# Optimization experiments

Hardware: AMD Instinct MI355X
Metric: run time of the kernel (lower is better)

Reference implementation:

```python
import math
import jax, jax.numpy as jnp
import numpy as np

IMG = 64  # configs['image_size']
EPS = 1e-8


def _bilinear_matrix(in_size, out_size):
    # Matches F.interpolate(mode='bilinear', align_corners=False) exactly,
    # including clamping of negative source coords and right-edge indices.
    scale = in_size / out_size
    src = (np.arange(out_size) + 0.5) * scale - 0.5
    src = np.clip(src, 0.0, in_size - 1)
    i0 = np.floor(src).astype(np.int64)
    i1 = np.minimum(i0 + 1, in_size - 1)
    w1 = (src - i0).astype(np.float32)
    W = np.zeros((out_size, in_size), dtype=np.float32)
    W[np.arange(out_size), i0] += (1.0 - w1)
    W[np.arange(out_size), i1] += w1
    return jnp.asarray(W)


def _resize(grids, out_size):
    # grids: [B, H, W] -> [B, out, out] via separable bilinear matrices (batched matmul)
    Wh = _bilinear_matrix(grids.shape[1], out_size)
    Ww = _bilinear_matrix(grids.shape[2], out_size)
    return jnp.einsum('oh,bhw,pw->bop', Wh, grids, Ww)


def _minmax(x):
    # global min-max over the whole [B,H,W] channel tensor (as in the torch code)
    lo, hi = x.min(), x.max()
    return jnp.where(hi - lo < EPS, jnp.zeros_like(x), (x - lo) / (hi - lo + EPS))


def _to_square_grid(vec):
    # vec: [B, L] -> [B, gs, gs] with zero padding (vectorized grid scatter)
    B, L = vec.shape
    gs = int(math.ceil(math.sqrt(L)))
    return jnp.pad(vec, ((0, 0), (0, gs * gs - L))).reshape(B, gs, gs)


def setup_inputs() -> dict:
    key = jax.random.key(0)
    hidden_state = jax.random.normal(key, (64, 512, 2048, 1), dtype=jnp.float32)
    return {"hidden_state": hidden_state}


def reference(hidden_state) -> jnp.ndarray:
    xs = hidden_state[..., 0]            # [B, E, N]

    # temporal view: mean over nodes -> [B, E] -> square grid -> bilinear resize
    temporal = _minmax(_resize(_to_square_grid(xs.mean(axis=2)), IMG))

    # spatial view: mean over embedding -> [B, N] -> square grid -> resize
    spatial = _minmax(_resize(_to_square_grid(xs.mean(axis=1)), IMG))

    # correlation view: row-normalized feature correlation [B, E, E] -> resize
    xc = xs - xs.mean(axis=2, keepdims=True)
    xn = xc / (jnp.linalg.norm(xc, axis=2, keepdims=True) + EPS)
    corr = jnp.einsum('ben,bfn->bef', xn, xn)
    correlation = _minmax(_resize(corr, IMG))

    return jnp.stack([temporal, spatial, correlation], axis=1)  # [B, 3, IMG, IMG]
```

## Files before the change

kernel.cpp:

```cpp
#include <hip/hip_runtime.h>
#include <math.h>

#define B_ 64
#define E_ 512
#define N_ 2048
#define EPSF 1e-8f

#define OFF_ROWMEAN 0
#define OFF_ROWINV  32768
#define OFF_COLSUM  65536
#define OFF_MM      196608
#define OFF_RAW     196616
#define OFF_ZPART   983048

__device__ __forceinline__ unsigned mapf(float x) {
    unsigned u = __float_as_uint(x);
    return (u & 0x80000000u) ? ~u : (u | 0x80000000u);
}
__device__ __forceinline__ float unmapf(unsigned m) {
    unsigned u = (m & 0x80000000u) ? (m ^ 0x80000000u) : ~m;
    return __uint_as_float(u);
}

__global__ __launch_bounds__(256) void k_rowstats(const float* __restrict__ x,
                                                  float* __restrict__ rowmean,
                                                  float* __restrict__ rowinv) {
    int b = blockIdx.y;
    int e = blockIdx.x * 4 + (threadIdx.x >> 6);
    int lane = threadIdx.x & 63;
    const float4* row = (const float4*)(x + ((size_t)b * E_ + e) * N_);
    float s = 0.f, sq = 0.f;
#pragma unroll
    for (int i = 0; i < 8; ++i) {
        float4 v = row[lane + 64 * i];
        s  += v.x + v.y + v.z + v.w;
        sq += v.x * v.x + v.y * v.y + v.z * v.z + v.w * v.w;
    }
#pragma unroll
    for (int m = 32; m; m >>= 1) {
        s  += __shfl_xor(s, m, 64);
        sq += __shfl_xor(sq, m, 64);
    }
    if (lane == 0) {
        float mean = s * (1.0f / N_);
        float var = sq - s * s * (1.0f / N_);
        if (var < 0.f) var = 0.f;
        rowmean[b * E_ + e] = mean;
        rowinv[b * E_ + e] = 1.0f / (sqrtf(var) + EPSF);
    }
}

__global__ __launch_bounds__(256) void k_colsum(const float* __restrict__ x,
                                                float* __restrict__ colsum) {
    int b = blockIdx.y;
    int nc = blockIdx.x & 7;
    int ec = blockIdx.x >> 3;
    int n = nc * 256 + threadIdx.x;
    const float* p = x + ((size_t)b * E_ + ec * 128) * N_ + n;
    float s = 0.f;
#pragma unroll 8
    for (int e = 0; e < 128; ++e) s += p[(size_t)e * N_];
    atomicAdd(&colsum[b * N_ + n], s);
}

__global__ __launch_bounds__(256) void k_z(const float* __restrict__ x,
                                           const float* __restrict__ rowmean,
                                           const float* __restrict__ rowinv,
                                           float* __restrict__ zpart) {
    __shared__ float yt[64 * 129];
    int b = blockIdx.x;
    int s = blockIdx.y;
    int k0 = s * 128;
    int t = threadIdx.x;

    int kk = t & 127;
    int oh = t >> 7;
    for (int oo = 0; oo < 64; oo += 2) {
        int o = oo + oh;
        int r0 = 8 * o + 3, r1 = 8 * o + 4;
        float m0 = rowmean[b * E_ + r0], i0 = rowinv[b * E_ + r0];
        float m1 = rowmean[b * E_ + r1], i1 = rowinv[b * E_ + r1];
        float a = x[((size_t)b * E_ + r0) * N_ + k0 + kk];
        float c = x[((size_t)b * E_ + r1) * N_ + k0 + kk];
        yt[o * 129 + kk] = 0.5f * ((a - m0) * i0 + (c - m1) * i1);
    }
    __syncthreads();

    int ti = t >> 4, tj = t & 15;
    float acc[4][4] = {};
#pragma unroll 4
    for (int k = 0; k < 128; ++k) {
        float ai[4], aj[4];
#pragma unroll
        for (int a = 0; a < 4; ++a) ai[a] = yt[(4 * ti + a) * 129 + k];
#pragma unroll
        for (int c = 0; c < 4; ++c) aj[c] = yt[(4 * tj + c) * 129 + k];
#pragma unroll
        for (int a = 0; a < 4; ++a)
#pragma unroll
            for (int c = 0; c < 4; ++c) acc[a][c] += ai[a] * aj[c];
    }
    float* zp = zpart + ((size_t)s * B_ + b) * 4096;
#pragma unroll
    for (int a = 0; a < 4; ++a)
#pragma unroll
        for (int c = 0; c < 4; ++c)
            zp[(4 * ti + a) * 64 + (4 * tj + c)] = acc[a][c];
}

__global__ __launch_bounds__(256) void k_views(const float* __restrict__ rowmean,
                                               const float* __restrict__ colsum,
                                               const float* __restrict__ zpart,
                                               float* __restrict__ raw,
                                               unsigned* __restrict__ mm) {
    int b = blockIdx.x, v = blockIdx.y;
    int t = threadIdx.x;
    __shared__ float g[2116];
    __shared__ int   ti0[64];
    __shared__ int   ti1[64];
    __shared__ float tw[64];
    __shared__ float smin[4], smax[4];

    int gs = (v == 0) ? 23 : 46;
    if (v < 2) {
        int L = (v == 0) ? 512 : 2048;
        int gg = gs * gs;
        const float* src = (v == 0) ? (rowmean + b * E_) : (colsum + b * N_);
        float sc = (v == 0) ? 1.0f : (1.0f / 512.0f);
        for (int i = t; i < gg; i += 256) g[i] = (i < L) ? src[i] * sc : 0.f;
        if (t < 64) {
            double scd = (double)gs / 64.0;
            double sp = ((double)t + 0.5) * scd - 0.5;
            if (sp < 0.0) sp = 0.0;
            double up = (double)(gs - 1);
            if (sp > up) sp = up;
            int i0 = (int)sp;
            ti0[t] = i0;
            ti1[t] = (i0 + 1 < gs) ? i0 + 1 : gs - 1;
            tw[t] = (float)(sp - (double)i0);
        }
    }
    __syncthreads();

    float lmin = INFINITY, lmax = -INFINITY;
    for (int it = 0; it < 16; ++it) {
        int pix = t + 256 * it;
        float val;
        if (v == 2) {
            val = 0.f;
#pragma unroll
            for (int s = 0; s < 16; ++s)
                val += zpart[((size_t)s * B_ + b) * 4096 + pix];
        } else {
            int o = pix >> 6, p = pix & 63;
            int i0 = ti0[o], i1 = ti1[o];
            float wh = tw[o];
            int j0 = ti0[p], j1 = ti1[p];
            float ww = tw[p];
            float top = g[i0 * gs + j0] * (1.f - ww) + g[i0 * gs + j1] * ww;
            float bot = g[i1 * gs + j0] * (1.f - ww) + g[i1 * gs + j1] * ww;
            val = top * (1.f - wh) + bot * wh;
        }
        raw[((size_t)b * 3 + v) * 4096 + pix] = val;
        lmin = fminf(lmin, val);
        lmax = fmaxf(lmax, val);
    }

    int lane = t & 63, wid = t >> 6;
#pragma unroll
    for (int m = 32; m; m >>= 1) {
        lmin = fminf(lmin, __shfl_xor(lmin, m, 64));
        lmax = fmaxf(lmax, __shfl_xor(lmax, m, 64));
    }
    if (lane == 0) { smin[wid] = lmin; smax[wid] = lmax; }
    __syncthreads();
    if (t == 0) {
        float mn = fminf(fminf(smin[0], smin[1]), fminf(smin[2], smin[3]));
        float mx = fmaxf(fmaxf(smax[0], smax[1]), fmaxf(smax[2], smax[3]));
        atomicMin(&mm[v], mapf(mn));
        atomicMax(&mm[3 + v], mapf(mx));
    }
}

__global__ __launch_bounds__(256) void k_norm(const float* __restrict__ raw,
                                              const unsigned* __restrict__ mm,
                                              float* __restrict__ out) {
    int b = blockIdx.x, v = blockIdx.y;
    int t = threadIdx.x;
    float lo = unmapf(mm[v]);
    float hi = unmapf(mm[3 + v]);
    float d = hi - lo;
    bool zero = (d < EPSF);
    float inv = 1.0f / (d + EPSF);
    size_t base = ((size_t)b * 3 + v) * 4096;
    for (int it = 0; it < 16; ++it) {
        int pix = t + 256 * it;
        float r = raw[base + pix];
        out[base + pix] = zero ? 0.f : (r - lo) * inv;
    }
}

extern "C" void kernel_launch(void* const* d_in, const int* in_sizes, int n_in,
                              void* d_out, int out_size, void* d_ws, size_t ws_size,
                              hipStream_t stream) {
    const float* x = (const float*)d_in[0];
    float* ws = (float*)d_ws;
    float* rowmean = ws + OFF_ROWMEAN;
    float* rowinv  = ws + OFF_ROWINV;
    float* colsum  = ws + OFF_COLSUM;
    unsigned* mm   = (unsigned*)(ws + OFF_MM);
    float* raw     = ws + OFF_RAW;
    float* zpart   = ws + OFF_ZPART;
    float* out     = (float*)d_out;

    hipMemsetAsync(colsum, 0, (size_t)B_ * N_ * sizeof(float), stream);
    hipMemsetAsync(mm, 0xFF, 3 * sizeof(unsigned), stream);
    hipMemsetAsync(mm + 3, 0x00, 3 * sizeof(unsigned), stream);

    k_rowstats<<<dim3(E_ / 4, B_), 256, 0, stream>>>(x, rowmean, rowinv);
    k_colsum<<<dim3(32, B_), 256, 0, stream>>>(x, colsum);
    k_z<<<dim3(B_, 16), 256, 0, stream>>>(x, rowmean, rowinv, zpart);
    k_views<<<dim3(B_, 3), 256, 0, stream>>>(rowmean, colsum, zpart, raw, mm);
    k_norm<<<dim3(B_, 3), 256, 0, stream>>>(raw, mm, out);
}
```

Measured before the change: 454.0 us.

## Fuse row stats and column sums into one pass; retile correlation GEMM per wavefront

```diff
diff --git a/kernel.cpp b/kernel.cpp
--- a/kernel.cpp
+++ b/kernel.cpp
@@ -8,10 +8,10 @@
 
 #define OFF_ROWMEAN 0
 #define OFF_ROWINV  32768
-#define OFF_COLSUM  65536
-#define OFF_MM      196608
-#define OFF_RAW     196616
-#define OFF_ZPART   983048
+#define OFF_COLPART 65536
+#define OFF_MM      2162688
+#define OFF_RAW     2162696
+#define OFF_ZPART   2949128
 
 __device__ __forceinline__ unsigned mapf(float x) {
     unsigned u = __float_as_uint(x);
@@ -22,94 +22,124 @@
     return __uint_as_float(u);
 }
 
-__global__ __launch_bounds__(256) void k_rowstats(const float* __restrict__ x,
-                                                  float* __restrict__ rowmean,
-                                                  float* __restrict__ rowinv) {
-    int b = blockIdx.y;
-    int e = blockIdx.x * 4 + (threadIdx.x >> 6);
-    int lane = threadIdx.x & 63;
-    const float4* row = (const float4*)(x + ((size_t)b * E_ + e) * N_);
-    float s = 0.f, sq = 0.f;
-#pragma unroll
-    for (int i = 0; i < 8; ++i) {
-        float4 v = row[lane + 64 * i];
-        s  += v.x + v.y + v.z + v.w;
-        sq += v.x * v.x + v.y * v.y + v.z * v.z + v.w * v.w;
-    }
-#pragma unroll
-    for (int m = 32; m; m >>= 1) {
-        s  += __shfl_xor(s, m, 64);
-        sq += __shfl_xor(sq, m, 64);
-    }
-    if (lane == 0) {
-        float mean = s * (1.0f / N_);
-        float var = sq - s * s * (1.0f / N_);
-        if (var < 0.f) var = 0.f;
-        rowmean[b * E_ + e] = mean;
-        rowinv[b * E_ + e] = 1.0f / (sqrtf(var) + EPSF);
-    }
-}
-
-__global__ __launch_bounds__(256) void k_colsum(const float* __restrict__ x,
-                                                float* __restrict__ colsum) {
-    int b = blockIdx.y;
-    int nc = blockIdx.x & 7;
-    int ec = blockIdx.x >> 3;
-    int n = nc * 256 + threadIdx.x;
-    const float* p = x + ((size_t)b * E_ + ec * 128) * N_ + n;
-    float s = 0.f;
-#pragma unroll 8
-    for (int e = 0; e < 128; ++e) s += p[(size_t)e * N_];
-    atomicAdd(&colsum[b * N_ + n], s);
-}
-
-__global__ __launch_bounds__(256) void k_z(const float* __restrict__ x,
-                                           const float* __restrict__ rowmean,
-                                           const float* __restrict__ rowinv,
-                                           float* __restrict__ zpart) {
-    __shared__ float yt[64 * 129];
+__global__ __launch_bounds__(256) void k_stats(const float* __restrict__ x,
+                                               float* __restrict__ rowmean,
+                                               float* __restrict__ rowinv,
+                                               float* __restrict__ colpart) {
+    __shared__ __align__(16) float cs[4][N_];
+    int b = blockIdx.y, ec = blockIdx.x;
+    int t = threadIdx.x, w = t >> 6, lane = t & 63;
+    float colacc[32];
+#pragma unroll
+    for (int i = 0; i < 32; ++i) colacc[i] = 0.f;
+    int ebase = ec * 32 + w * 8;
+#pragma unroll 1
+    for (int r = 0; r < 8; ++r) {
+        int e = ebase + r;
+        const float4* row = (const float4*)(x + ((size_t)b * E_ + e) * N_);
+        float s = 0.f, sq = 0.f;
+#pragma unroll
+        for (int i = 0; i < 8; ++i) {
+            float4 v = row[lane + 64 * i];
+            s += v.x + v.y + v.z + v.w;
+            sq = fmaf(v.x, v.x, sq);
+            sq = fmaf(v.y, v.y, sq);
+            sq = fmaf(v.z, v.z, sq);
+            sq = fmaf(v.w, v.w, sq);
+            colacc[4 * i + 0] += v.x;
+            colacc[4 * i + 1] += v.y;
+            colacc[4 * i + 2] += v.z;
+            colacc[4 * i + 3] += v.w;
+        }
+#pragma unroll
+        for (int m = 32; m; m >>= 1) {
+            s += __shfl_xor(s, m, 64);
+            sq += __shfl_xor(sq, m, 64);
+        }
+        if (lane == 0) {
+            float mean = s * (1.0f / N_);
+            float var = sq - s * s * (1.0f / N_);
+            if (var < 0.f) var = 0.f;
+            rowmean[b * E_ + e] = mean;
+            rowinv[b * E_ + e] = 1.0f / (sqrtf(var) + EPSF);
+        }
+    }
+    float4* slice = (float4*)cs[w];
+#pragma unroll
+    for (int i = 0; i < 8; ++i)
+        slice[lane + 64 * i] = make_float4(colacc[4 * i], colacc[4 * i + 1],
+                                           colacc[4 * i + 2], colacc[4 * i + 3]);
+    __syncthreads();
+    float* cp = colpart + ((size_t)ec * B_ + b) * N_;
+    for (int c = t; c < N_; c += 256)
+        cp[c] = cs[0][c] + cs[1][c] + cs[2][c] + cs[3][c];
+}
+
+__global__ __launch_bounds__(64) void k_z(const float* __restrict__ x,
+                                          const float* __restrict__ rowmean,
+                                          const float* __restrict__ rowinv,
+                                          float* __restrict__ zpart) {
+    __shared__ __align__(16) float Y[64 * 128];
     int b = blockIdx.x;
-    int s = blockIdx.y;
-    int k0 = s * 128;
-    int t = threadIdx.x;
-
-    int kk = t & 127;
-    int oh = t >> 7;
-    for (int oo = 0; oo < 64; oo += 2) {
-        int o = oo + oh;
+    int kc = blockIdx.y;
+    int k0 = kc * 128;
+    int lane = threadIdx.x;
+    const float* xb = x + (size_t)b * E_ * N_;
+    const float* rm = rowmean + b * E_;
+    const float* ri = rowinv + b * E_;
+    int mg = lane >> 1;
+    int jj = (lane & 1) * 2;
+#pragma unroll 4
+    for (int o = 0; o < 64; ++o) {
         int r0 = 8 * o + 3, r1 = 8 * o + 4;
-        float m0 = rowmean[b * E_ + r0], i0 = rowinv[b * E_ + r0];
-        float m1 = rowmean[b * E_ + r1], i1 = rowinv[b * E_ + r1];
-        float a = x[((size_t)b * E_ + r0) * N_ + k0 + kk];
-        float c = x[((size_t)b * E_ + r1) * N_ + k0 + kk];
-        yt[o * 129 + kk] = 0.5f * ((a - m0) * i0 + (c - m1) * i1);
-    }
-    __syncthreads();
-
-    int ti = t >> 4, tj = t & 15;
-    float acc[4][4] = {};
-#pragma unroll 4
-    for (int k = 0; k < 128; ++k) {
-        float ai[4], aj[4];
-#pragma unroll
-        for (int a = 0; a < 4; ++a) ai[a] = yt[(4 * ti + a) * 129 + k];
-#pragma unroll
-        for (int c = 0; c < 4; ++c) aj[c] = yt[(4 * tj + c) * 129 + k];
-#pragma unroll
-        for (int a = 0; a < 4; ++a)
-#pragma unroll
-            for (int c = 0; c < 4; ++c) acc[a][c] += ai[a] * aj[c];
-    }
-    float* zp = zpart + ((size_t)s * B_ + b) * 4096;
-#pragma unroll
-    for (int a = 0; a < 4; ++a)
-#pragma unroll
-        for (int c = 0; c < 4; ++c)
-            zp[(4 * ti + a) * 64 + (4 * tj + c)] = acc[a][c];
+        float2 a = *(const float2*)(xb + (size_t)r0 * N_ + k0 + 2 * lane);
+        float2 c = *(const float2*)(xb + (size_t)r1 * N_ + k0 + 2 * lane);
+        float m0 = rm[r0], s0 = ri[r0];
+        float m1 = rm[r1], s1 = ri[r1];
+        float2 yv;
+        yv.x = 0.5f * ((a.x - m0) * s0 + (c.x - m1) * s1);
+        yv.y = 0.5f * ((a.y - m0) * s0 + (c.y - m1) * s1);
+        *(float2*)&Y[o * 128 + 4 * (mg ^ (o >> 3)) + jj] = yv;
+    }
+    __syncthreads();
+
+    int ti = lane >> 3, tj = lane & 7;
+    float acc[8][8];
+#pragma unroll
+    for (int i = 0; i < 8; ++i)
+#pragma unroll
+        for (int j = 0; j < 8; ++j) acc[i][j] = 0.f;
+
+#pragma unroll 2
+    for (int m4 = 0; m4 < 32; ++m4) {
+        float4 av[8], bv[8];
+#pragma unroll
+        for (int a = 0; a < 8; ++a)
+            av[a] = *(const float4*)&Y[(8 * ti + a) * 128 + 4 * (m4 ^ ti)];
+#pragma unroll
+        for (int c = 0; c < 8; ++c)
+            bv[c] = *(const float4*)&Y[(8 * tj + c) * 128 + 4 * (m4 ^ tj)];
+#pragma unroll
+        for (int a = 0; a < 8; ++a)
+#pragma unroll
+            for (int c = 0; c < 8; ++c) {
+                acc[a][c] = fmaf(av[a].x, bv[c].x, acc[a][c]);
+                acc[a][c] = fmaf(av[a].y, bv[c].y, acc[a][c]);
+                acc[a][c] = fmaf(av[a].z, bv[c].z, acc[a][c]);
+                acc[a][c] = fmaf(av[a].w, bv[c].w, acc[a][c]);
+            }
+    }
+    float* zp = zpart + ((size_t)kc * B_ + b) * 4096;
+#pragma unroll
+    for (int a = 0; a < 8; ++a) {
+        int rr = (8 * ti + a) * 64 + 8 * tj;
+        *(float4*)&zp[rr]     = make_float4(acc[a][0], acc[a][1], acc[a][2], acc[a][3]);
+        *(float4*)&zp[rr + 4] = make_float4(acc[a][4], acc[a][5], acc[a][6], acc[a][7]);
+    }
 }
 
 __global__ __launch_bounds__(256) void k_views(const float* __restrict__ rowmean,
-                                               const float* __restrict__ colsum,
+                                               const float* __restrict__ colpart,
                                                const float* __restrict__ zpart,
                                                float* __restrict__ raw,
                                                unsigned* __restrict__ mm) {
@@ -125,9 +155,20 @@
     if (v < 2) {
         int L = (v == 0) ? 512 : 2048;
         int gg = gs * gs;
-        const float* src = (v == 0) ? (rowmean + b * E_) : (colsum + b * N_);
-        float sc = (v == 0) ? 1.0f : (1.0f / 512.0f);
-        for (int i = t; i < gg; i += 256) g[i] = (i < L) ? src[i] * sc : 0.f;
+        for (int i = t; i < gg; i += 256) {
+            float val = 0.f;
+            if (i < L) {
+                if (v == 0) {
+                    val = rowmean[b * E_ + i];
+                } else {
+#pragma unroll
+                    for (int ch = 0; ch < 16; ++ch)
+                        val += colpart[((size_t)ch * B_ + b) * N_ + i];
+                    val *= (1.0f / 512.0f);
+                }
+            }
+            g[i] = val;
+        }
         if (t < 64) {
             double scd = (double)gs / 64.0;
             double sp = ((double)t + 0.5) * scd - 0.5;
@@ -207,19 +248,17 @@
     float* ws = (float*)d_ws;
     float* rowmean = ws + OFF_ROWMEAN;
     float* rowinv  = ws + OFF_ROWINV;
-    float* colsum  = ws + OFF_COLSUM;
+    float* colpart = ws + OFF_COLPART;
     unsigned* mm   = (unsigned*)(ws + OFF_MM);
     float* raw     = ws + OFF_RAW;
     float* zpart   = ws + OFF_ZPART;
     float* out     = (float*)d_out;
 
-    hipMemsetAsync(colsum, 0, (size_t)B_ * N_ * sizeof(float), stream);
     hipMemsetAsync(mm, 0xFF, 3 * sizeof(unsigned), stream);
     hipMemsetAsync(mm + 3, 0x00, 3 * sizeof(unsigned), stream);
 
-    k_rowstats<<<dim3(E_ / 4, B_), 256, 0, stream>>>(x, rowmean, rowinv);
-    k_colsum<<<dim3(32, B_), 256, 0, stream>>>(x, colsum);
-    k_z<<<dim3(B_, 16), 256, 0, stream>>>(x, rowmean, rowinv, zpart);
-    k_views<<<dim3(B_, 3), 256, 0, stream>>>(rowmean, colsum, zpart, raw, mm);
+    k_stats<<<dim3(16, B_), 256, 0, stream>>>(x, rowmean, rowinv, colpart);
+    k_z<<<dim3(B_, 16), 64, 0, stream>>>(x, rowmean, rowinv, zpart);
+    k_views<<<dim3(B_, 3), 256, 0, stream>>>(rowmean, colpart, zpart, raw, mm);
     k_norm<<<dim3(B_, 3), 256, 0, stream>>>(raw, mm, out);
 }
```

Measured after the change: 416.6 us. -8.2%, faster.
